# Optimization experiments

Hardware: AMD Instinct MI355X
Metric: run time of the kernel (lower is better)

The kernel has to match this reference:

```python
import jax, jax.numpy as jnp
import numpy as np

B, S, D = 2, 1024, 1024
H = 4 * D          # SwiGLU hidden
E = 8              # routed experts
K = 2              # top_k
NS = 1             # shared experts


def setup_inputs() -> dict:
    key = jax.random.key(0)
    ks = jax.random.split(key, 8)
    sc = 0.02  # init scale for stability
    return {
        "x": jax.random.normal(ks[0], (B, S, D), jnp.float32),
        "shared_w1": jax.random.normal(ks[1], (NS, D, H), jnp.float32) * sc,
        "shared_w2": jax.random.normal(ks[2], (NS, D, H), jnp.float32) * sc,
        "shared_w3": jax.random.normal(ks[3], (NS, H, D), jnp.float32) * sc,
        "w1": jax.random.normal(ks[4], (E, D, H), jnp.float32) * sc,
        "w2": jax.random.normal(ks[5], (E, D, H), jnp.float32) * sc,
        "w3": jax.random.normal(ks[6], (E, H, D), jnp.float32) * sc,
        "router_w": jax.random.normal(ks[7], (E, D), jnp.float32) * sc,
    }


def _experts(xf, W1, W2, W3):
    # xf: [T, D]; W1,W2: [E, D, H]; W3: [E, H, D] -> [E, T, D]
    h = jax.nn.silu(jnp.einsum("td,edh->eth", xf, W1)) * jnp.einsum("td,edh->eth", xf, W2)
    return jnp.einsum("eth,ehd->etd", h, W3)


def reference(x, shared_w1, shared_w2, shared_w3, w1, w2, w3, router_w):
    b, s, d = x.shape
    xf = x.reshape(-1, d)                       # [T, D]
    T = xf.shape[0]

    # shared experts (summed over NS experts)
    shared_out = _experts(xf, shared_w1, shared_w2, shared_w3).sum(axis=0)  # [T, D]

    # router: nn.Linear(dim, E, bias=False) => x @ W^T
    logits = jnp.einsum("td,ed->te", xf, router_w)   # [T, E]
    probs = jax.nn.softmax(logits, axis=1)
    topw, topi = jax.lax.top_k(probs, K)             # [T, K]
    topw = topw / topw.sum(axis=-1, keepdims=True)

    # dense combine-weight matrix [T, E]: zero except at selected experts
    cw = jnp.zeros((T, E), x.dtype).at[jnp.arange(T)[:, None], topi].add(topw)

    # all-expert outputs, weighted combine (faithful to masked loop + scatter-add)
    y = _experts(xf, w1, w2, w3)                     # [E, T, D]
    routed = jnp.einsum("te,etd->td", cw, y)         # [T, D]

    out = (shared_out + routed).reshape(b, s, d)
    return (out, logits)
```

## Files before the change

### kernel.cpp

```cpp
#include <hip/hip_runtime.h>


#define TD 2048
#define DD 1024
#define HH 4096
#define NEXP 8
#define LDAH 40

typedef _Float16 f16x8 __attribute__((ext_vector_type(8)));
typedef _Float16 f16x4 __attribute__((ext_vector_type(4)));
typedef float f32x4 __attribute__((ext_vector_type(4)));

#define WS_COUNTS   0
#define WS_CURS     64
#define WS_HBASE    128
#define WS_TOKLIST  256
#define WS_TOKW     65792
#define WS_TOPI     131328
#define WS_TOPW     147712
#define WS_H        262144
#define WS_WT       (262144 + 58720256)

__global__ __launch_bounds__(256) void k_router(const float* __restrict__ x,
    const float* __restrict__ rw, float* __restrict__ logits,
    int* __restrict__ topi, float* __restrict__ topw, int* __restrict__ counts) {
  int wv = threadIdx.x >> 6, lane = threadIdx.x & 63;
  int t = blockIdx.x * 4 + wv;
  const float* xt = x + (size_t)t * DD;
  float lg[NEXP];
#pragma unroll
  for (int e = 0; e < NEXP; ++e) {
    const float* we = rw + e * DD;
    float acc = 0.f;
#pragma unroll
    for (int j = 0; j < DD / 64; ++j) acc += xt[j * 64 + lane] * we[j * 64 + lane];
#pragma unroll
    for (int off = 32; off; off >>= 1) acc += __shfl_xor(acc, off);
    lg[e] = acc;
  }
  if (lane == 0) {
    float m = lg[0];
#pragma unroll
    for (int e = 1; e < NEXP; ++e) m = fmaxf(m, lg[e]);
    float p[NEXP];
#pragma unroll
    for (int e = 0; e < NEXP; ++e) p[e] = __expf(lg[e] - m);
    int i0 = 0; float p0 = p[0];
#pragma unroll
    for (int e = 1; e < NEXP; ++e) if (p[e] > p0) { p0 = p[e]; i0 = e; }
    int i1 = -1; float p1 = -1.f;
#pragma unroll
    for (int e = 0; e < NEXP; ++e) if (e != i0 && p[e] > p1) { p1 = p[e]; i1 = e; }
    float wsum = p0 + p1;
#pragma unroll
    for (int e = 0; e < NEXP; ++e) logits[t * NEXP + e] = lg[e];
    topi[t * 2] = i0; topi[t * 2 + 1] = i1;
    topw[t * 2] = p0 / wsum; topw[t * 2 + 1] = p1 / wsum;
    atomicAdd(&counts[i0], 1); atomicAdd(&counts[i1], 1);
  }
}

__global__ void k_offsets(const int* __restrict__ counts, int* __restrict__ hbase) {
  if (threadIdx.x == 0) {
    int base = TD;
    for (int e = 0; e < NEXP; ++e) { hbase[e] = base; base += (counts[e] + 127) & ~127; }
  }
}

__global__ void k_scatter(const int* __restrict__ topi, const float* __restrict__ topw,
                          int* __restrict__ curs, int* __restrict__ tokl, float* __restrict__ tokw) {
  int tid = blockIdx.x * 256 + threadIdx.x;
  if (tid >= TD * 2) return;
  int e = topi[tid];
  int pos = atomicAdd(&curs[e], 1);
  tokl[e * TD + pos] = tid >> 1;
  tokw[e * TD + pos] = topw[tid];
}

__device__ __forceinline__ void transpose_tile(const float* __restrict__ src,
    _Float16* __restrict__ dst, int R, int C, int r0, int c0) {
  __shared__ _Float16 tile[64][68];
  int t = threadIdx.x;
#pragma unroll
  for (int i = 0; i < 4; ++i) {
    int r = (t >> 4) + i * 16;
    int c = (t & 15) * 4;
    float4 v = *(const float4*)(src + (size_t)(r0 + r) * C + c0 + c);
    *(f16x4*)&tile[r][c] = (f16x4){(_Float16)v.x, (_Float16)v.y, (_Float16)v.z, (_Float16)v.w};
  }
  __syncthreads();
#pragma unroll
  for (int i = 0; i < 2; ++i) {
    int cc = (t >> 3) + i * 32;
    int rr = (t & 7) * 8;
    f16x8 hv;
#pragma unroll
    for (int j = 0; j < 8; ++j) hv[j] = tile[rr + j][cc];
    *(f16x8*)(dst + (size_t)(c0 + cc) * R + r0 + rr) = hv;
  }
}

__global__ __launch_bounds__(256) void k_tr1(const float* __restrict__ sw1, const float* __restrict__ sw2,
    const float* __restrict__ w1, const float* __restrict__ w2, _Float16* __restrict__ wt) {
  int id = blockIdx.y;
  const float* src = (id == 0) ? sw1 : (id == 1) ? sw2
                   : (id < 10) ? w1 + (size_t)(id - 2) * DD * HH
                               : w2 + (size_t)(id - 10) * DD * HH;
  _Float16* dst = wt + (size_t)id * DD * HH;
  transpose_tile(src, dst, DD, HH, (blockIdx.x >> 6) * 64, (blockIdx.x & 63) * 64);
}

__global__ __launch_bounds__(256) void k_tr2(const float* __restrict__ sw3,
    const float* __restrict__ w3, _Float16* __restrict__ wt) {
  int id = blockIdx.y;
  const float* src = (id == 0) ? sw3 : w3 + (size_t)(id - 1) * HH * DD;
  _Float16* dst = wt + (size_t)id * HH * DD;
  transpose_tile(src, dst, HH, DD, (blockIdx.x >> 4) * 64, (blockIdx.x & 15) * 64);
}

__global__ __launch_bounds__(256, 2) void k_gemm1(
    const float* __restrict__ x, const _Float16* __restrict__ wt,
    const int* __restrict__ counts, const int* __restrict__ hbase,
    const int* __restrict__ tok_list, _Float16* __restrict__ h) {
  __shared__ _Float16 lA[128 * LDAH];
  __shared__ _Float16 lB1[128 * LDAH];
  __shared__ _Float16 lB2[128 * LDAH];
  __shared__ int stok[128];

  int slot = blockIdx.y;
  const _Float16 *w1t, *w2t;
  int hrow0;
  if (slot < 16) {
    w1t = wt;
    w2t = wt + (size_t)1 * DD * HH;
    hrow0 = slot * 128;
  } else {
    int e = (slot - 16) >> 4, rt = (slot - 16) & 15;
    if (rt * 128 >= counts[e]) return;
    w1t = wt + (size_t)(2 + e) * DD * HH;
    w2t = wt + (size_t)(10 + e) * DD * HH;
    hrow0 = hbase[e] + rt * 128;
  }
  if (threadIdx.x < 128) {
    int tok;
    if (slot < 16) tok = hrow0 + threadIdx.x;
    else {
      int e = (slot - 16) >> 4, rt = (slot - 16) & 15;
      tok = tok_list[e * TD + rt * 128 + threadIdx.x];
    }
    stok[threadIdx.x] = tok;
  }

  int n0 = blockIdx.x * 128;
  int wv = threadIdx.x >> 6, lane = threadIdx.x & 63;
  int wm = (wv & 1) * 64, wn = (wv >> 1) * 64;
  f32x4 acc1[4][4] = {}; f32x4 acc2[4][4] = {};

  for (int kk = 0; kk < DD; kk += 32) {
    __syncthreads();
    {
      int r = threadIdx.x >> 3;
      int c = (threadIdx.x & 7) * 4;
#pragma unroll
      for (int i = 0; i < 4; ++i) {
        int row = r + i * 32;
        float4 v = *(const float4*)(x + (size_t)stok[row] * DD + kk + c);
        *(f16x4*)&lA[row * LDAH + c] = (f16x4){(_Float16)v.x, (_Float16)v.y, (_Float16)v.z, (_Float16)v.w};
      }
    }
    {
      int rr = lane >> 2;
      int seg = (lane & 3) * 8;
#pragma unroll
      for (int j = 0; j < 4; ++j) {
        int task = wv + j * 4;
        int mat = task >> 3, it = task & 7;
        int row = it * 16 + rr;
        const _Float16* src = (mat ? w2t : w1t) + (size_t)(n0 + row) * DD + kk + seg;
        _Float16* dst = (mat ? lB2 : lB1) + row * LDAH + seg;
        *(f16x8*)dst = *(const f16x8*)src;
      }
    }
    __syncthreads();
    f16x8 af[4];
    int rA = lane & 15, g = (lane >> 4) * 8;
#pragma unroll
    for (int mi = 0; mi < 4; ++mi)
      af[mi] = *(const f16x8*)&lA[(wm + mi * 16 + rA) * LDAH + g];
#pragma unroll
    for (int ni = 0; ni < 4; ++ni) {
      f16x8 b1 = *(const f16x8*)&lB1[(wn + ni * 16 + rA) * LDAH + g];
      f16x8 b2 = *(const f16x8*)&lB2[(wn + ni * 16 + rA) * LDAH + g];
#pragma unroll
      for (int mi = 0; mi < 4; ++mi) {
        acc1[mi][ni] = __builtin_amdgcn_mfma_f32_16x16x32_f16(af[mi], b1, acc1[mi][ni], 0, 0, 0);
        acc2[mi][ni] = __builtin_amdgcn_mfma_f32_16x16x32_f16(af[mi], b2, acc2[mi][ni], 0, 0, 0);
      }
    }
  }
#pragma unroll
  for (int mi = 0; mi < 4; ++mi) {
#pragma unroll
    for (int ni = 0; ni < 4; ++ni) {
#pragma unroll
      for (int i = 0; i < 4; ++i) {
        int r = wm + mi * 16 + (lane >> 4) * 4 + i;
        int c = wn + ni * 16 + (lane & 15);
        float a = acc1[mi][ni][i], b = acc2[mi][ni][i];
        float hv = (a / (1.f + __expf(-a))) * b;
        h[(size_t)(hrow0 + r) * HH + n0 + c] = (_Float16)hv;
      }
    }
  }
}

__global__ __launch_bounds__(256, 2) void k_gemm2(
    const _Float16* __restrict__ h, const _Float16* __restrict__ wt,
    const int* __restrict__ counts, const int* __restrict__ hbase,
    const int* __restrict__ tok_list, const float* __restrict__ tok_w,
    float* __restrict__ out) {
  __shared__ _Float16 lA[128 * LDAH];
  __shared__ _Float16 lB[128 * LDAH];
  __shared__ int stok[128];
  __shared__ float swt[128];

  int slot = blockIdx.y;
  const _Float16* w3t;
  int hrow0, cnt;
  if (slot < 16) {
    w3t = wt;
    hrow0 = slot * 128; cnt = 128;
  } else {
    int e = (slot - 16) >> 4, rt = (slot - 16) & 15;
    cnt = counts[e] - rt * 128;
    if (cnt <= 0) return;
    if (cnt > 128) cnt = 128;
    w3t = wt + (size_t)(1 + e) * HH * DD;
    hrow0 = hbase[e] + rt * 128;
  }
  if (threadIdx.x < 128) {
    int tok; float w;
    if (slot < 16) { tok = hrow0 + threadIdx.x; w = 1.f; }
    else {
      int e = (slot - 16) >> 4, rt = (slot - 16) & 15;
      int idx = rt * 128 + threadIdx.x;
      tok = tok_list[e * TD + idx]; w = tok_w[e * TD + idx];
    }
    stok[threadIdx.x] = tok; swt[threadIdx.x] = w;
  }

  int n0 = blockIdx.x * 128;
  int kz0 = blockIdx.z * (HH / 2);
  int wv = threadIdx.x >> 6, lane = threadIdx.x & 63;
  int wm = (wv & 1) * 64, wn = (wv >> 1) * 64;
  f32x4 acc[4][4] = {};

  for (int kk = kz0; kk < kz0 + HH / 2; kk += 32) {
    __syncthreads();
    {
      int rr = lane >> 2;
      int seg = (lane & 3) * 8;
#pragma unroll
      for (int j = 0; j < 4; ++j) {
        int task = wv + j * 4;
        int mat = task >> 3, it = task & 7;
        int row = it * 16 + rr;
        const _Float16* src = mat ? (w3t + (size_t)(n0 + row) * HH + kk + seg)
                                  : (h + (size_t)(hrow0 + row) * HH + kk + seg);
        _Float16* dst = (mat ? lB : lA) + row * LDAH + seg;
        *(f16x8*)dst = *(const f16x8*)src;
      }
    }
    __syncthreads();
    f16x8 af[4];
    int rA = lane & 15, g = (lane >> 4) * 8;
#pragma unroll
    for (int mi = 0; mi < 4; ++mi)
      af[mi] = *(const f16x8*)&lA[(wm + mi * 16 + rA) * LDAH + g];
#pragma unroll
    for (int ni = 0; ni < 4; ++ni) {
      f16x8 bf = *(const f16x8*)&lB[(wn + ni * 16 + rA) * LDAH + g];
#pragma unroll
      for (int mi = 0; mi < 4; ++mi)
        acc[mi][ni] = __builtin_amdgcn_mfma_f32_16x16x32_f16(af[mi], bf, acc[mi][ni], 0, 0, 0);
    }
  }
#pragma unroll
  for (int mi = 0; mi < 4; ++mi) {
#pragma unroll
    for (int i = 0; i < 4; ++i) {
      int r = wm + mi * 16 + (lane >> 4) * 4 + i;
      if (r < cnt) {
        int tok = stok[r]; float w = swt[r];
#pragma unroll
        for (int ni = 0; ni < 4; ++ni) {
          int c = wn + ni * 16 + (lane & 15);
          atomicAdd(&out[(size_t)tok * DD + n0 + c], w * acc[mi][ni][i]);
        }
      }
    }
  }
}

extern "C" void kernel_launch(void* const* d_in, const int* in_sizes, int n_in,
                              void* d_out, int out_size, void* d_ws, size_t ws_size,
                              hipStream_t stream) {
  const float* x   = (const float*)d_in[0];
  const float* sw1 = (const float*)d_in[1];
  const float* sw2 = (const float*)d_in[2];
  const float* sw3 = (const float*)d_in[3];
  const float* w1  = (const float*)d_in[4];
  const float* w2  = (const float*)d_in[5];
  const float* w3  = (const float*)d_in[6];
  const float* rw  = (const float*)d_in[7];
  float* out = (float*)d_out;
  char* ws = (char*)d_ws;

  int*   counts = (int*)(ws + WS_COUNTS);
  int*   curs   = (int*)(ws + WS_CURS);
  int*   hbase  = (int*)(ws + WS_HBASE);
  int*   tokl   = (int*)(ws + WS_TOKLIST);
  float* tokw   = (float*)(ws + WS_TOKW);
  int*   topi   = (int*)(ws + WS_TOPI);
  float* topw   = (float*)(ws + WS_TOPW);
  _Float16* hbuf = (_Float16*)(ws + WS_H);
  _Float16* wt   = (_Float16*)(ws + WS_WT);

  hipMemsetAsync(ws, 0, WS_TOKLIST + 65536, stream);
  hipMemsetAsync(out, 0, (size_t)TD * DD * sizeof(float), stream);

  k_router<<<TD / 4, 256, 0, stream>>>(x, rw, out + (size_t)TD * DD, topi, topw, counts);
  k_offsets<<<1, 64, 0, stream>>>(counts, hbase);
  k_scatter<<<16, 256, 0, stream>>>(topi, topw, curs, tokl, tokw);

  k_tr1<<<dim3(1024, 18), 256, 0, stream>>>(sw1, sw2, w1, w2, wt);
  k_gemm1<<<dim3(HH / 128, 144), 256, 0, stream>>>(x, wt, counts, hbase, tokl, hbuf);
  k_tr2<<<dim3(1024, 9), 256, 0, stream>>>(sw3, w3, wt);
  k_gemm2<<<dim3(DD / 128, 144, 2), 256, 0, stream>>>(hbuf, wt, counts, hbase, tokl, tokw, out);
}
```

Before: 834.8 us.

## Use direct global-to-LDS loads with swizzled tiles and replace atomic combine with gather pass

Pre-converts x to fp16 once, then both GEMMs load A and B tiles with global_load_lds 16-byte direct-to-LDS transfers into an unpadded, XOR-swizzled 32-column layout in place of register-staged copies. GEMM2 no longer scatters weighted results with float atomics. It writes per-split fp16 partial outputs to buffers reused from the weight workspace, and a new combine kernel gathers the shared and two routed rows per token using recorded positions. This removes atomic contention and the output memset, at the cost of an extra kernel, extra fp16 traffic, and fp16 rounding of partial sums.

```diff
diff --git a/kernel.cpp b/kernel.cpp
--- a/kernel.cpp
+++ b/kernel.cpp
@@ -5,7 +5,6 @@
 #define DD 1024
 #define HH 4096
 #define NEXP 8
-#define LDAH 40
 
 typedef _Float16 f16x8 __attribute__((ext_vector_type(8)));
 typedef _Float16 f16x4 __attribute__((ext_vector_type(4)));
@@ -15,11 +14,32 @@
 #define WS_CURS     64
 #define WS_HBASE    128
 #define WS_TOKLIST  256
-#define WS_TOKW     65792
-#define WS_TOPI     131328
-#define WS_TOPW     147712
-#define WS_H        262144
-#define WS_WT       (262144 + 58720256)
+#define WS_TOPI     65792
+#define WS_TOPW     82176
+#define WS_POS      98560
+#define WS_XH       131072
+#define WS_H        4325376
+#define WS_WT       63045632
+#define WTSLOT      ((size_t)DD * HH)
+
+typedef __attribute__((address_space(3))) void lds_void;
+typedef const __attribute__((address_space(1))) void gbl_void;
+__device__ __forceinline__ void gld16(void* l, const void* g) {
+  __builtin_amdgcn_global_load_lds((gbl_void*)g, (lds_void*)l, 16, 0, 0);
+}
+
+__device__ __forceinline__ f16x8 frag_ld(const _Float16* tile, int r, int qsel) {
+  int q = qsel ^ ((r >> 1) & 3);
+  return *(const f16x8*)((const char*)tile + r * 64 + q * 16);
+}
+
+__global__ __launch_bounds__(256) void k_xh(const float* __restrict__ x, _Float16* __restrict__ xh) {
+  int i = (blockIdx.x * 256 + threadIdx.x) * 8;
+  float4 a = *(const float4*)(x + i), b = *(const float4*)(x + i + 4);
+  f16x8 v = {(_Float16)a.x, (_Float16)a.y, (_Float16)a.z, (_Float16)a.w,
+             (_Float16)b.x, (_Float16)b.y, (_Float16)b.z, (_Float16)b.w};
+  *(f16x8*)(xh + i) = v;
+}
 
 __global__ __launch_bounds__(256) void k_router(const float* __restrict__ x,
     const float* __restrict__ rw, float* __restrict__ logits,
@@ -67,14 +87,14 @@
   }
 }
 
-__global__ void k_scatter(const int* __restrict__ topi, const float* __restrict__ topw,
-                          int* __restrict__ curs, int* __restrict__ tokl, float* __restrict__ tokw) {
+__global__ void k_scatter(const int* __restrict__ topi, int* __restrict__ curs,
+                          int* __restrict__ tokl, int* __restrict__ posarr) {
   int tid = blockIdx.x * 256 + threadIdx.x;
   if (tid >= TD * 2) return;
   int e = topi[tid];
   int pos = atomicAdd(&curs[e], 1);
   tokl[e * TD + pos] = tid >> 1;
-  tokw[e * TD + pos] = topw[tid];
+  posarr[tid] = pos;
 }
 
 __device__ __forceinline__ void transpose_tile(const float* __restrict__ src,
@@ -106,7 +126,7 @@
   const float* src = (id == 0) ? sw1 : (id == 1) ? sw2
                    : (id < 10) ? w1 + (size_t)(id - 2) * DD * HH
                                : w2 + (size_t)(id - 10) * DD * HH;
-  _Float16* dst = wt + (size_t)id * DD * HH;
+  _Float16* dst = wt + (size_t)id * WTSLOT;
   transpose_tile(src, dst, DD, HH, (blockIdx.x >> 6) * 64, (blockIdx.x & 63) * 64);
 }
 
@@ -114,83 +134,74 @@
     const float* __restrict__ w3, _Float16* __restrict__ wt) {
   int id = blockIdx.y;
   const float* src = (id == 0) ? sw3 : w3 + (size_t)(id - 1) * HH * DD;
-  _Float16* dst = wt + (size_t)id * HH * DD;
+  _Float16* dst = wt + (size_t)id * WTSLOT;
   transpose_tile(src, dst, HH, DD, (blockIdx.x >> 4) * 64, (blockIdx.x & 15) * 64);
 }
 
 __global__ __launch_bounds__(256, 2) void k_gemm1(
-    const float* __restrict__ x, const _Float16* __restrict__ wt,
+    const _Float16* __restrict__ xh, const _Float16* __restrict__ wt,
     const int* __restrict__ counts, const int* __restrict__ hbase,
     const int* __restrict__ tok_list, _Float16* __restrict__ h) {
-  __shared__ _Float16 lA[128 * LDAH];
-  __shared__ _Float16 lB1[128 * LDAH];
-  __shared__ _Float16 lB2[128 * LDAH];
+  __shared__ _Float16 lA[128 * 32];
+  __shared__ _Float16 lB1[128 * 32];
+  __shared__ _Float16 lB2[128 * 32];
   __shared__ int stok[128];
 
   int slot = blockIdx.y;
   const _Float16 *w1t, *w2t;
   int hrow0;
   if (slot < 16) {
-    w1t = wt;
-    w2t = wt + (size_t)1 * DD * HH;
-    hrow0 = slot * 128;
+    w1t = wt; w2t = wt + WTSLOT; hrow0 = slot * 128;
   } else {
     int e = (slot - 16) >> 4, rt = (slot - 16) & 15;
     if (rt * 128 >= counts[e]) return;
-    w1t = wt + (size_t)(2 + e) * DD * HH;
-    w2t = wt + (size_t)(10 + e) * DD * HH;
+    w1t = wt + (size_t)(2 + e) * WTSLOT;
+    w2t = wt + (size_t)(10 + e) * WTSLOT;
     hrow0 = hbase[e] + rt * 128;
   }
   if (threadIdx.x < 128) {
-    int tok;
-    if (slot < 16) tok = hrow0 + threadIdx.x;
-    else {
-      int e = (slot - 16) >> 4, rt = (slot - 16) & 15;
-      tok = tok_list[e * TD + rt * 128 + threadIdx.x];
-    }
+    int tok = (slot < 16) ? (hrow0 + threadIdx.x)
+                          : tok_list[((slot - 16) >> 4) * TD + ((slot - 16) & 15) * 128 + threadIdx.x];
     stok[threadIdx.x] = tok;
   }
+  __syncthreads();
 
   int n0 = blockIdx.x * 128;
   int wv = threadIdx.x >> 6, lane = threadIdx.x & 63;
   int wm = (wv & 1) * 64, wn = (wv >> 1) * 64;
+  int qsel = lane >> 4;
+
+  const _Float16 *gA[2], *gB1[2], *gB2[2];
+  int ldsoff[2];
+#pragma unroll
+  for (int jj = 0; jj < 2; ++jj) {
+    int j = wv * 2 + jj;
+    int n = j * 16 + (lane >> 2);
+    int q = (lane & 3) ^ ((n >> 1) & 3);
+    gA[jj]  = xh + (size_t)stok[n] * DD + q * 8;
+    gB1[jj] = w1t + (size_t)(n0 + n) * DD + q * 8;
+    gB2[jj] = w2t + (size_t)(n0 + n) * DD + q * 8;
+    ldsoff[jj] = j * 1024 + lane * 16;
+  }
+
   f32x4 acc1[4][4] = {}; f32x4 acc2[4][4] = {};
 
   for (int kk = 0; kk < DD; kk += 32) {
     __syncthreads();
-    {
-      int r = threadIdx.x >> 3;
-      int c = (threadIdx.x & 7) * 4;
-#pragma unroll
-      for (int i = 0; i < 4; ++i) {
-        int row = r + i * 32;
-        float4 v = *(const float4*)(x + (size_t)stok[row] * DD + kk + c);
-        *(f16x4*)&lA[row * LDAH + c] = (f16x4){(_Float16)v.x, (_Float16)v.y, (_Float16)v.z, (_Float16)v.w};
-      }
-    }
-    {
-      int rr = lane >> 2;
-      int seg = (lane & 3) * 8;
-#pragma unroll
-      for (int j = 0; j < 4; ++j) {
-        int task = wv + j * 4;
-        int mat = task >> 3, it = task & 7;
-        int row = it * 16 + rr;
-        const _Float16* src = (mat ? w2t : w1t) + (size_t)(n0 + row) * DD + kk + seg;
-        _Float16* dst = (mat ? lB2 : lB1) + row * LDAH + seg;
-        *(f16x8*)dst = *(const f16x8*)src;
-      }
+#pragma unroll
+    for (int jj = 0; jj < 2; ++jj) {
+      gld16((char*)lA + ldsoff[jj], gA[jj] + kk);
+      gld16((char*)lB1 + ldsoff[jj], gB1[jj] + kk);
+      gld16((char*)lB2 + ldsoff[jj], gB2[jj] + kk);
     }
     __syncthreads();
     f16x8 af[4];
-    int rA = lane & 15, g = (lane >> 4) * 8;
-#pragma unroll
-    for (int mi = 0; mi < 4; ++mi)
-      af[mi] = *(const f16x8*)&lA[(wm + mi * 16 + rA) * LDAH + g];
+#pragma unroll
+    for (int mi = 0; mi < 4; ++mi) af[mi] = frag_ld(lA, wm + mi * 16 + (lane & 15), qsel);
 #pragma unroll
     for (int ni = 0; ni < 4; ++ni) {
-      f16x8 b1 = *(const f16x8*)&lB1[(wn + ni * 16 + rA) * LDAH + g];
-      f16x8 b2 = *(const f16x8*)&lB2[(wn + ni * 16 + rA) * LDAH + g];
+      f16x8 b1 = frag_ld(lB1, wn + ni * 16 + (lane & 15), qsel);
+      f16x8 b2 = frag_ld(lB2, wn + ni * 16 + (lane & 15), qsel);
 #pragma unroll
       for (int mi = 0; mi < 4; ++mi) {
         acc1[mi][ni] = __builtin_amdgcn_mfma_f32_16x16x32_f16(af[mi], b1, acc1[mi][ni], 0, 0, 0);
@@ -199,107 +210,110 @@
     }
   }
 #pragma unroll
-  for (int mi = 0; mi < 4; ++mi) {
-#pragma unroll
-    for (int ni = 0; ni < 4; ++ni) {
+  for (int mi = 0; mi < 4; ++mi)
+#pragma unroll
+    for (int ni = 0; ni < 4; ++ni)
 #pragma unroll
       for (int i = 0; i < 4; ++i) {
         int r = wm + mi * 16 + (lane >> 4) * 4 + i;
         int c = wn + ni * 16 + (lane & 15);
         float a = acc1[mi][ni][i], b = acc2[mi][ni][i];
-        float hv = (a / (1.f + __expf(-a))) * b;
-        h[(size_t)(hrow0 + r) * HH + n0 + c] = (_Float16)hv;
+        h[(size_t)(hrow0 + r) * HH + n0 + c] = (_Float16)((a / (1.f + __expf(-a))) * b);
       }
-    }
-  }
 }
 
 __global__ __launch_bounds__(256, 2) void k_gemm2(
     const _Float16* __restrict__ h, const _Float16* __restrict__ wt,
     const int* __restrict__ counts, const int* __restrict__ hbase,
-    const int* __restrict__ tok_list, const float* __restrict__ tok_w,
-    float* __restrict__ out) {
-  __shared__ _Float16 lA[128 * LDAH];
-  __shared__ _Float16 lB[128 * LDAH];
-  __shared__ int stok[128];
-  __shared__ float swt[128];
+    _Float16* __restrict__ y0, _Float16* __restrict__ y1) {
+  __shared__ _Float16 lA[128 * 32];
+  __shared__ _Float16 lB[128 * 32];
 
   int slot = blockIdx.y;
   const _Float16* w3t;
-  int hrow0, cnt;
+  int hrow0;
   if (slot < 16) {
-    w3t = wt;
-    hrow0 = slot * 128; cnt = 128;
+    w3t = wt; hrow0 = slot * 128;
   } else {
     int e = (slot - 16) >> 4, rt = (slot - 16) & 15;
-    cnt = counts[e] - rt * 128;
-    if (cnt <= 0) return;
-    if (cnt > 128) cnt = 128;
-    w3t = wt + (size_t)(1 + e) * HH * DD;
+    if (rt * 128 >= counts[e]) return;
+    w3t = wt + (size_t)(1 + e) * WTSLOT;
     hrow0 = hbase[e] + rt * 128;
   }
-  if (threadIdx.x < 128) {
-    int tok; float w;
-    if (slot < 16) { tok = hrow0 + threadIdx.x; w = 1.f; }
-    else {
-      int e = (slot - 16) >> 4, rt = (slot - 16) & 15;
-      int idx = rt * 128 + threadIdx.x;
-      tok = tok_list[e * TD + idx]; w = tok_w[e * TD + idx];
-    }
-    stok[threadIdx.x] = tok; swt[threadIdx.x] = w;
-  }
+  _Float16* y = blockIdx.z ? y1 : y0;
+  int kz0 = blockIdx.z * (HH / 2);
 
   int n0 = blockIdx.x * 128;
-  int kz0 = blockIdx.z * (HH / 2);
   int wv = threadIdx.x >> 6, lane = threadIdx.x & 63;
   int wm = (wv & 1) * 64, wn = (wv >> 1) * 64;
+  int qsel = lane >> 4;
+
+  const _Float16 *gA[2], *gB[2];
+  int ldsoff[2];
+#pragma unroll
+  for (int jj = 0; jj < 2; ++jj) {
+    int j = wv * 2 + jj;
+    int n = j * 16 + (lane >> 2);
+    int q = (lane & 3) ^ ((n >> 1) & 3);
+    gA[jj] = h   + (size_t)(hrow0 + n) * HH + kz0 + q * 8;
+    gB[jj] = w3t + (size_t)(n0 + n)   * HH + kz0 + q * 8;
+    ldsoff[jj] = j * 1024 + lane * 16;
+  }
+
   f32x4 acc[4][4] = {};
-
-  for (int kk = kz0; kk < kz0 + HH / 2; kk += 32) {
+  for (int kk = 0; kk < HH / 2; kk += 32) {
     __syncthreads();
-    {
-      int rr = lane >> 2;
-      int seg = (lane & 3) * 8;
-#pragma unroll
-      for (int j = 0; j < 4; ++j) {
-        int task = wv + j * 4;
-        int mat = task >> 3, it = task & 7;
-        int row = it * 16 + rr;
-        const _Float16* src = mat ? (w3t + (size_t)(n0 + row) * HH + kk + seg)
-                                  : (h + (size_t)(hrow0 + row) * HH + kk + seg);
-        _Float16* dst = (mat ? lB : lA) + row * LDAH + seg;
-        *(f16x8*)dst = *(const f16x8*)src;
-      }
+#pragma unroll
+    for (int jj = 0; jj < 2; ++jj) {
+      gld16((char*)lA + ldsoff[jj], gA[jj] + kk);
+      gld16((char*)lB + ldsoff[jj], gB[jj] + kk);
     }
     __syncthreads();
     f16x8 af[4];
-    int rA = lane & 15, g = (lane >> 4) * 8;
-#pragma unroll
-    for (int mi = 0; mi < 4; ++mi)
-      af[mi] = *(const f16x8*)&lA[(wm + mi * 16 + rA) * LDAH + g];
+#pragma unroll
+    for (int mi = 0; mi < 4; ++mi) af[mi] = frag_ld(lA, wm + mi * 16 + (lane & 15), qsel);
 #pragma unroll
     for (int ni = 0; ni < 4; ++ni) {
-      f16x8 bf = *(const f16x8*)&lB[(wn + ni * 16 + rA) * LDAH + g];
+      f16x8 bf = frag_ld(lB, wn + ni * 16 + (lane & 15), qsel);
 #pragma unroll
       for (int mi = 0; mi < 4; ++mi)
         acc[mi][ni] = __builtin_amdgcn_mfma_f32_16x16x32_f16(af[mi], bf, acc[mi][ni], 0, 0, 0);
     }
   }
 #pragma unroll
-  for (int mi = 0; mi < 4; ++mi) {
-#pragma unroll
-    for (int i = 0; i < 4; ++i) {
-      int r = wm + mi * 16 + (lane >> 4) * 4 + i;
-      if (r < cnt) {
-        int tok = stok[r]; float w = swt[r];
-#pragma unroll
-        for (int ni = 0; ni < 4; ++ni) {
-          int c = wn + ni * 16 + (lane & 15);
-          atomicAdd(&out[(size_t)tok * DD + n0 + c], w * acc[mi][ni][i]);
-        }
+  for (int mi = 0; mi < 4; ++mi)
+#pragma unroll
+    for (int ni = 0; ni < 4; ++ni)
+#pragma unroll
+      for (int i = 0; i < 4; ++i) {
+        int r = wm + mi * 16 + (lane >> 4) * 4 + i;
+        int c = wn + ni * 16 + (lane & 15);
+        y[(size_t)(hrow0 + r) * DD + n0 + c] = (_Float16)acc[mi][ni][i];
       }
-    }
-  }
+}
+
+__global__ __launch_bounds__(256) void k_combine(
+    const _Float16* __restrict__ y0, const _Float16* __restrict__ y1,
+    const int* __restrict__ topi, const float* __restrict__ topw,
+    const int* __restrict__ posarr, const int* __restrict__ hbase,
+    float* __restrict__ out) {
+  int t = blockIdx.x;
+  int c = threadIdx.x * 4;
+  int e0 = topi[2 * t], e1 = topi[2 * t + 1];
+  float w0 = topw[2 * t], w1 = topw[2 * t + 1];
+  size_t rs = (size_t)t * DD + c;
+  size_t r0 = (size_t)(hbase[e0] + posarr[2 * t]) * DD + c;
+  size_t r1 = (size_t)(hbase[e1] + posarr[2 * t + 1]) * DD + c;
+  f16x4 s0 = *(const f16x4*)(y0 + rs), s1 = *(const f16x4*)(y1 + rs);
+  f16x4 a0 = *(const f16x4*)(y0 + r0), a1 = *(const f16x4*)(y1 + r0);
+  f16x4 b0 = *(const f16x4*)(y0 + r1), b1 = *(const f16x4*)(y1 + r1);
+  float4 o;
+  float* op = &o.x;
+#pragma unroll
+  for (int i = 0; i < 4; ++i)
+    op[i] = (float)s0[i] + (float)s1[i] + w0 * ((float)a0[i] + (float)a1[i])
+          + w1 * ((float)b0[i] + (float)b1[i]);
+  *(float4*)(out + rs) = o;
 }
 
 extern "C" void kernel_launch(void* const* d_in, const int* in_sizes, int n_in,
@@ -320,21 +334,25 @@
   int*   curs   = (int*)(ws + WS_CURS);
   int*   hbase  = (int*)(ws + WS_HBASE);
   int*   tokl   = (int*)(ws + WS_TOKLIST);
-  float* tokw   = (float*)(ws + WS_TOKW);
   int*   topi   = (int*)(ws + WS_TOPI);
   float* topw   = (float*)(ws + WS_TOPW);
+  int*   posarr = (int*)(ws + WS_POS);
+  _Float16* xh   = (_Float16*)(ws + WS_XH);
   _Float16* hbuf = (_Float16*)(ws + WS_H);
   _Float16* wt   = (_Float16*)(ws + WS_WT);
-
-  hipMemsetAsync(ws, 0, WS_TOKLIST + 65536, stream);
-  hipMemsetAsync(out, 0, (size_t)TD * DD * sizeof(float), stream);
-
+  _Float16* ybuf0 = wt + 9 * WTSLOT;
+  _Float16* ybuf1 = wt + 11 * WTSLOT;
+
+  hipMemsetAsync(ws, 0, 65792, stream);
+
+  k_xh<<<TD * DD / 2048, 256, 0, stream>>>(x, xh);
   k_router<<<TD / 4, 256, 0, stream>>>(x, rw, out + (size_t)TD * DD, topi, topw, counts);
   k_offsets<<<1, 64, 0, stream>>>(counts, hbase);
-  k_scatter<<<16, 256, 0, stream>>>(topi, topw, curs, tokl, tokw);
+  k_scatter<<<16, 256, 0, stream>>>(topi, curs, tokl, posarr);
 
   k_tr1<<<dim3(1024, 18), 256, 0, stream>>>(sw1, sw2, w1, w2, wt);
-  k_gemm1<<<dim3(HH / 128, 144), 256, 0, stream>>>(x, wt, counts, hbase, tokl, hbuf);
+  k_gemm1<<<dim3(HH / 128, 144), 256, 0, stream>>>(xh, wt, counts, hbase, tokl, hbuf);
   k_tr2<<<dim3(1024, 9), 256, 0, stream>>>(sw3, w3, wt);
-  k_gemm2<<<dim3(DD / 128, 144, 2), 256, 0, stream>>>(hbuf, wt, counts, hbase, tokl, tokw, out);
-}
+  k_gemm2<<<dim3(DD / 128, 144, 2), 256, 0, stream>>>(hbuf, wt, counts, hbase, ybuf0, ybuf1);
+  k_combine<<<TD, 256, 0, stream>>>(ybuf0, ybuf1, topi, topw, posarr, hbase, out);
+}
```

Result: faster. 794.7 us (-4.8%).
